# Kernel tuning notes

Hardware: AMD Instinct MI355X
Metric: run time of the kernel (lower is better)

## Reference

```python
import jax, jax.numpy as jnp
import numpy as np

N_TOKENS = 65536
EMBED_DIM = 1024
NUM_EXPERTS = 8
TOP_K = 2
NOISE_EPS = 0.2


def setup_inputs() -> dict:
    key = jax.random.key(0)
    k_x, k_eps, k_wg, k_wn = jax.random.split(key, 4)
    x = jax.random.normal(k_x, (N_TOKENS, EMBED_DIM), dtype=jnp.float32)
    eps = jax.random.normal(k_eps, (N_TOKENS, NUM_EXPERTS), dtype=jnp.float32)
    # nn.init.normal_(std=1.0) on both weights
    w_gate = jax.random.normal(k_wg, (EMBED_DIM, NUM_EXPERTS), dtype=jnp.float32)
    w_noise = jax.random.normal(k_wn, (EMBED_DIM, NUM_EXPERTS), dtype=jnp.float32)
    return {"x": x, "eps": eps, "w_gate": w_gate, "w_noise": w_noise}


def reference(x, eps, w_gate, w_noise):
    # skinny GEMMs: [N, D] @ [D, E] -> [N, E]
    clean_logits = x @ w_gate
    raw_noise_stddev = x @ w_noise
    noise_stddev = jax.nn.softplus(raw_noise_stddev) + NOISE_EPS
    noisy_logits = clean_logits + noise_stddev * eps

    # top-k over the tiny expert dim, softmax over the k selected logits
    top_k_logits, indices = jax.lax.top_k(noisy_logits, TOP_K)  # [N, K]
    top_k_gates = jax.nn.softmax(top_k_logits, axis=-1)

    # scatter gates back into dense [N, E]
    n = noisy_logits.shape[0]
    rows = jnp.arange(n)[:, None]
    gates = jnp.zeros_like(noisy_logits).at[rows, indices].set(top_k_gates)

    # load-balancing aux loss
    probs = jax.nn.softmax(clean_logits, axis=-1)
    P = probs.mean(axis=0)                             # [E]
    f = (gates > 0).astype(x.dtype).mean(axis=0)       # [E]
    aux_loss = NUM_EXPERTS * jnp.sum(P * f)
    return gates, aux_loss
```

## Files before the change

### kernel.cpp

```cpp
#include <hip/hip_runtime.h>
#include <math.h>


#define N_TOKENS   65536
#define EMBED_DIM  1024
#define NE         8
#define BROWS      64
#define CHUNK      64
#define NCHUNK     (EMBED_DIM / CHUNK)
#define QSTRIDE    260
#define NSLOT      64
#define NOISE_EPS  0.2f

#define AS1(p) (const __attribute__((address_space(1))) void*)(p)
#define AS3(p) (__attribute__((address_space(3))) void*)(p)

__global__ __launch_bounds__(256, 4)
void router_kernel(const float* __restrict__ x,
                   const float* __restrict__ eps,
                   const float* __restrict__ wg,
                   const float* __restrict__ wn,
                   float* __restrict__ gates,
                   float* __restrict__ acc ) {
    __shared__ float tile[2][16 * QSTRIDE];

    const int t    = threadIdx.x;
    const int lane = t & 63;
    const int w    = __builtin_amdgcn_readfirstlane(t >> 6);
    const long rowbase = (long)blockIdx.x * BROWS;
    const int  c0 = blockIdx.x & (NCHUNK - 1);

    const int srow = lane >> 4;
    const int scol = (lane & 15) * 4;

    const int tb = (lane >> 2) * QSTRIDE + (lane & 3) * 64 + w * 16;

    float accg[NE], accn[NE];
#pragma unroll
    for (int e = 0; e < NE; ++e) { accg[e] = 0.f; accn[e] = 0.f; }

#pragma unroll
    for (int cc = 0; cc < 2; ++cc) {
        const int ca = (c0 + cc) & (NCHUNK - 1);
#pragma unroll
        for (int i = 0; i < 4; ++i) {
            const int q = w * 4 + i;
            const float* gp = x + (rowbase + q * 4 + srow) * (long)EMBED_DIM
                              + ca * CHUNK + scol;
            __builtin_amdgcn_global_load_lds(AS1(gp), AS3(&tile[cc][q * QSTRIDE]),
                                             16, 0, 0);
        }
    }

#pragma unroll 1
    for (int c = 0; c < NCHUNK; ++c) {
        const int b  = c & 1;
        const int ca = (c0 + c) & (NCHUNK - 1);

        if (c == NCHUNK - 1) asm volatile("s_waitcnt vmcnt(0)" ::: "memory");
        else                 asm volatile("s_waitcnt vmcnt(4)" ::: "memory");
        __builtin_amdgcn_s_barrier();
        asm volatile("" ::: "memory");

        float4 xv[4];
#pragma unroll
        for (int j = 0; j < 4; ++j)
            xv[j] = *(const float4*)&tile[b][tb + j * 4];
        asm volatile("s_waitcnt lgkmcnt(0)" ::: "memory");
        __builtin_amdgcn_sched_barrier(0);
        __builtin_amdgcn_s_barrier();
        asm volatile("" ::: "memory");

        if (c + 2 < NCHUNK) {
            const int can = (c0 + c + 2) & (NCHUNK - 1);
#pragma unroll
            for (int i = 0; i < 4; ++i) {
                const int q = w * 4 + i;
                const float* gp = x + (rowbase + q * 4 + srow) * (long)EMBED_DIM
                                  + can * CHUNK + scol;
                __builtin_amdgcn_global_load_lds(AS1(gp),
                                                 AS3(&tile[b][q * QSTRIDE]),
                                                 16, 0, 0);
            }
        }

        const float* wgc = wg + ((long)ca * CHUNK + w * 16) * NE;
        const float* wnc = wn + ((long)ca * CHUNK + w * 16) * NE;
#pragma unroll
        for (int j = 0; j < 4; ++j) {
            const float xa[4] = { xv[j].x, xv[j].y, xv[j].z, xv[j].w };
#pragma unroll
            for (int q = 0; q < 4; ++q) {
                const int k = j * 4 + q;
#pragma unroll
                for (int e = 0; e < NE; ++e) {
                    accg[e] = fmaf(xa[q], wgc[k * NE + e], accg[e]);
                    accn[e] = fmaf(xa[q], wnc[k * NE + e], accn[e]);
                }
            }
        }
    }

    float* part = (float*)tile;
    if (w != 0) {
#pragma unroll
        for (int e = 0; e < NE; ++e) {
            part[((w - 1) * BROWS + lane) * 16 + e]      = accg[e];
            part[((w - 1) * BROWS + lane) * 16 + NE + e] = accn[e];
        }
    }
    __syncthreads();
    if (w != 0) return;

#pragma unroll
    for (int v = 0; v < 3; ++v)
#pragma unroll
        for (int e = 0; e < NE; ++e) {
            accg[e] += part[(v * BROWS + lane) * 16 + e];
            accn[e] += part[(v * BROWS + lane) * 16 + NE + e];
        }

    const long row = rowbase + lane;
    const float* er = eps + row * NE;
    float4 ev0 = *(const float4*)(er);
    float4 ev1 = *(const float4*)(er + 4);
    float epsv[NE] = { ev0.x, ev0.y, ev0.z, ev0.w, ev1.x, ev1.y, ev1.z, ev1.w };

    float noisy[NE];
#pragma unroll
    for (int e = 0; e < NE; ++e) {
        float r = accn[e];
        float sp = fmaxf(r, 0.f) + log1pf(expf(-fabsf(r)));
        noisy[e] = accg[e] + (sp + NOISE_EPS) * epsv[e];
    }

    int i1 = 0; float v1 = noisy[0];
#pragma unroll
    for (int e = 1; e < NE; ++e) if (noisy[e] > v1) { v1 = noisy[e]; i1 = e; }
    int i2 = -1; float v2 = -INFINITY;
#pragma unroll
    for (int e = 0; e < NE; ++e) if (e != i1 && noisy[e] > v2) { v2 = noisy[e]; i2 = e; }

    float bb = expf(v2 - v1);
    float g2 = bb / (1.f + bb);
    float g1 = 1.f - g2;

    float* gr = gates + row * NE;
    float ov[NE];
#pragma unroll
    for (int e = 0; e < NE; ++e)
        ov[e] = (e == i1) ? g1 : ((e == i2) ? g2 : 0.f);
    *(float4*)(gr)     = make_float4(ov[0], ov[1], ov[2], ov[3]);
    *(float4*)(gr + 4) = make_float4(ov[4], ov[5], ov[6], ov[7]);

    float mx = accg[0];
#pragma unroll
    for (int e = 1; e < NE; ++e) mx = fmaxf(mx, accg[e]);
    float p[NE]; float s = 0.f;
#pragma unroll
    for (int e = 0; e < NE; ++e) { p[e] = expf(accg[e] - mx); s += p[e]; }
    float inv = 1.f / s;

    float vals[16];
#pragma unroll
    for (int e = 0; e < NE; ++e) {
        vals[e]      = p[e] * inv;
        vals[NE + e] = ((i1 == e) ? 1.f : 0.f) + ((i2 == e && g2 > 0.f) ? 1.f : 0.f);
    }
#pragma unroll
    for (int off = 32; off > 0; off >>= 1)
#pragma unroll
        for (int i = 0; i < 16; ++i)
            vals[i] += __shfl_xor(vals[i], off, 64);

    if (lane == 0) {
        float* slot = acc + (blockIdx.x & (NSLOT - 1)) * 16;
#pragma unroll
        for (int i = 0; i < 16; ++i)
            atomicAdd(&slot[i], vals[i]);
    }
}

__global__ void finalize_kernel(const float* __restrict__ acc,
                                float* __restrict__ out_aux) {
    __shared__ float s[16];
    const int t = threadIdx.x;
    if (t < 16) {
        float v = 0.f;
        for (int j = 0; j < NSLOT; ++j) v += acc[j * 16 + t];
        s[t] = v;
    }
    __syncthreads();
    if (t == 0) {
        const float invn = 1.f / (float)N_TOKENS;
        float aux = 0.f;
#pragma unroll
        for (int e = 0; e < NE; ++e)
            aux += (s[e] * invn) * (s[NE + e] * invn);
        *out_aux = (float)NE * aux;
    }
}

extern "C" void kernel_launch(void* const* d_in, const int* in_sizes, int n_in,
                              void* d_out, int out_size, void* d_ws, size_t ws_size,
                              hipStream_t stream) {
    const float* x   = (const float*)d_in[0];
    const float* eps = (const float*)d_in[1];
    const float* wg  = (const float*)d_in[2];
    const float* wn  = (const float*)d_in[3];
    float* out = (float*)d_out;
    float* acc = (float*)d_ws;

    hipMemsetAsync(d_ws, 0, NSLOT * 16 * sizeof(float), stream);

    router_kernel<<<dim3(N_TOKENS / BROWS), dim3(256), 0, stream>>>(
        x, eps, wg, wn, out, acc);
    finalize_kernel<<<dim3(1), dim3(64), 0, stream>>>(acc, out + (out_size - 1));
}
```

Before: 378.9 us.

## Double chunk width, use 512-thread blocks, and XOR-swizzle the LDS tile

Doubles the K-chunk staged per iteration to 128 columns and uses 8 waves per block, each reducing over 16 columns. The LDS tile drops its padded stride in favour of an XOR swizzle of the column groups, applied both when global_load_lds writes and when threads read back, to avoid bank conflicts. The aim is more memory-level parallelism per block and half as many barrier iterations. In exchange, LDS use per block roughly doubles, which may limit occupancy, and the final cross-wave reduction grows from 3 to 7 partials.

New measurement: 379.2 us. No clear change (+0.1%).

```diff
diff --git a/kernel.cpp b/kernel.cpp
--- a/kernel.cpp
+++ b/kernel.cpp
@@ -6,23 +6,24 @@
 #define EMBED_DIM  1024
 #define NE         8
 #define BROWS      64
-#define CHUNK      64
+#define CHUNK      128
 #define NCHUNK     (EMBED_DIM / CHUNK)
-#define QSTRIDE    260
+#define QSTRIDE    512
+#define BUFSZ      (16 * QSTRIDE)
 #define NSLOT      64
 #define NOISE_EPS  0.2f
 
 #define AS1(p) (const __attribute__((address_space(1))) void*)(p)
 #define AS3(p) (__attribute__((address_space(3))) void*)(p)
 
-__global__ __launch_bounds__(256, 4)
+__global__ __launch_bounds__(512, 4)
 void router_kernel(const float* __restrict__ x,
                    const float* __restrict__ eps,
                    const float* __restrict__ wg,
                    const float* __restrict__ wn,
                    float* __restrict__ gates,
                    float* __restrict__ acc ) {
-    __shared__ float tile[2][16 * QSTRIDE];
+    __shared__ float tile[2][BUFSZ];
 
     const int t    = threadIdx.x;
     const int lane = t & 63;
@@ -31,9 +32,14 @@
     const int  c0 = blockIdx.x & (NCHUNK - 1);
 
     const int srow = lane >> 4;
-    const int scol = (lane & 15) * 4;
-
-    const int tb = (lane >> 2) * QSTRIDE + (lane & 3) * 64 + w * 16;
+    const int pgr  = lane & 15;
+
+    const int g = lane >> 2;
+    const int tbase = g * QSTRIDE + (w >> 2) * 256 + (lane & 3) * 64;
+    int off[4];
+#pragma unroll
+    for (int j = 0; j < 4; ++j)
+        off[j] = ((((w & 3) * 4 + j) ^ (g & 7)) << 2);
 
     float accg[NE], accn[NE];
 #pragma unroll
@@ -43,12 +49,15 @@
     for (int cc = 0; cc < 2; ++cc) {
         const int ca = (c0 + cc) & (NCHUNK - 1);
 #pragma unroll
-        for (int i = 0; i < 4; ++i) {
-            const int q = w * 4 + i;
-            const float* gp = x + (rowbase + q * 4 + srow) * (long)EMBED_DIM
-                              + ca * CHUNK + scol;
-            __builtin_amdgcn_global_load_lds(AS1(gp), AS3(&tile[cc][q * QSTRIDE]),
-                                             16, 0, 0);
+        for (int i = 0; i < 2; ++i) {
+            const int q = w * 2 + i;
+#pragma unroll
+            for (int j = 0; j < 2; ++j) {
+                const int col = ca * CHUNK + j * 64 + ((pgr ^ (q & 7)) << 2);
+                const float* gp = x + (rowbase + q * 4 + srow) * (long)EMBED_DIM + col;
+                __builtin_amdgcn_global_load_lds(AS1(gp),
+                    AS3(&tile[cc][q * QSTRIDE + j * 256]), 16, 0, 0);
+            }
         }
     }
 
@@ -65,7 +74,7 @@
         float4 xv[4];
 #pragma unroll
         for (int j = 0; j < 4; ++j)
-            xv[j] = *(const float4*)&tile[b][tb + j * 4];
+            xv[j] = *(const float4*)&tile[b][tbase + off[j]];
         asm volatile("s_waitcnt lgkmcnt(0)" ::: "memory");
         __builtin_amdgcn_sched_barrier(0);
         __builtin_amdgcn_s_barrier();
@@ -74,13 +83,15 @@
         if (c + 2 < NCHUNK) {
             const int can = (c0 + c + 2) & (NCHUNK - 1);
 #pragma unroll
-            for (int i = 0; i < 4; ++i) {
-                const int q = w * 4 + i;
-                const float* gp = x + (rowbase + q * 4 + srow) * (long)EMBED_DIM
-                                  + can * CHUNK + scol;
-                __builtin_amdgcn_global_load_lds(AS1(gp),
-                                                 AS3(&tile[b][q * QSTRIDE]),
-                                                 16, 0, 0);
+            for (int i = 0; i < 2; ++i) {
+                const int q = w * 2 + i;
+#pragma unroll
+                for (int j = 0; j < 2; ++j) {
+                    const int col = can * CHUNK + j * 64 + ((pgr ^ (q & 7)) << 2);
+                    const float* gp = x + (rowbase + q * 4 + srow) * (long)EMBED_DIM + col;
+                    __builtin_amdgcn_global_load_lds(AS1(gp),
+                        AS3(&tile[b][q * QSTRIDE + j * 256]), 16, 0, 0);
+                }
             }
         }
 
@@ -90,12 +101,12 @@
         for (int j = 0; j < 4; ++j) {
             const float xa[4] = { xv[j].x, xv[j].y, xv[j].z, xv[j].w };
 #pragma unroll
-            for (int q = 0; q < 4; ++q) {
-                const int k = j * 4 + q;
+            for (int qi = 0; qi < 4; ++qi) {
+                const int k = j * 4 + qi;
 #pragma unroll
                 for (int e = 0; e < NE; ++e) {
-                    accg[e] = fmaf(xa[q], wgc[k * NE + e], accg[e]);
-                    accn[e] = fmaf(xa[q], wnc[k * NE + e], accn[e]);
+                    accg[e] = fmaf(xa[qi], wgc[k * NE + e], accg[e]);
+                    accn[e] = fmaf(xa[qi], wnc[k * NE + e], accn[e]);
                 }
             }
         }
@@ -113,7 +124,7 @@
     if (w != 0) return;
 
 #pragma unroll
-    for (int v = 0; v < 3; ++v)
+    for (int v = 0; v < 7; ++v)
 #pragma unroll
         for (int e = 0; e < NE; ++e) {
             accg[e] += part[(v * BROWS + lane) * 16 + e];
@@ -168,10 +179,10 @@
         vals[NE + e] = ((i1 == e) ? 1.f : 0.f) + ((i2 == e && g2 > 0.f) ? 1.f : 0.f);
     }
 #pragma unroll
-    for (int off = 32; off > 0; off >>= 1)
+    for (int off2 = 32; off2 > 0; off2 >>= 1)
 #pragma unroll
         for (int i = 0; i < 16; ++i)
-            vals[i] += __shfl_xor(vals[i], off, 64);
+            vals[i] += __shfl_xor(vals[i], off2, 64);
 
     if (lane == 0) {
         float* slot = acc + (blockIdx.x & (NSLOT - 1)) * 16;
@@ -213,7 +224,7 @@
 
     hipMemsetAsync(d_ws, 0, NSLOT * 16 * sizeof(float), stream);
 
-    router_kernel<<<dim3(N_TOKENS / BROWS), dim3(256), 0, stream>>>(
+    router_kernel<<<dim3(N_TOKENS / BROWS), dim3(512), 0, stream>>>(
         x, eps, wg, wn, out, acc);
     finalize_kernel<<<dim3(1), dim3(64), 0, stream>>>(acc, out + (out_size - 1));
 }
```
